# Kernel tuning notes

Measured on AMD Instinct MI355X. Metric: run time of the kernel, lower is better.

Reference implementation:

```python
import jax, jax.numpy as jnp
import numpy as np

HID = 256   # hidden_dim
P = 16      # pool_size
EPS = 1e-5


def _ln(x, g, b):
    m = x.mean(-1, keepdims=True)
    v = x.var(-1, keepdims=True)
    return (x - m) * jax.lax.rsqrt(v + EPS) * g + b


def setup_inputs() -> dict:
    key = jax.random.key(0)
    ks = jax.random.split(key, 12)
    B, Cf, H, W = 8, 512, 64, 64
    Cg = Cf // 2
    Co = Cf // 2
    s = 0.02
    d = {}
    d['e_f'] = jax.random.normal(ks[0], (B, Cf, H, W), jnp.float32)
    d['e_g'] = jax.random.normal(ks[1], (B, Cg, H, W), jnp.float32)
    d['l_feat'] = jax.random.normal(ks[2], (B, 768, 20), jnp.float32)
    d['l_mask'] = jnp.ones((B, 20, 1), jnp.float32)
    d['ln_f_g'] = jnp.ones((Cf,), jnp.float32)
    d['ln_f_b'] = jnp.zeros((Cf,), jnp.float32)
    d['ln_g_g'] = jnp.ones((Cg,), jnp.float32)
    d['ln_g_b'] = jnp.zeros((Cg,), jnp.float32)
    d['wq'] = jax.random.normal(ks[3], (Cf, HID), jnp.float32) * s
    d['bq'] = jnp.zeros((HID,), jnp.float32)
    d['wk'] = jax.random.normal(ks[4], (Cg, HID), jnp.float32) * s
    d['bk'] = jnp.zeros((HID,), jnp.float32)
    d['wv'] = jax.random.normal(ks[5], (Cg, HID), jnp.float32) * s
    d['bv'] = jnp.zeros((HID,), jnp.float32)
    d['wo'] = jax.random.normal(ks[6], (HID, HID), jnp.float32) * s
    d['bo'] = jnp.zeros((HID,), jnp.float32)
    d['dw_k'] = jax.random.normal(ks[7], (HID, 1, 3, 3), jnp.float32) * s  # depthwise kernel (OIHW, I=1)
    d['efp_w'] = jax.random.normal(ks[8], (HID, Cf), jnp.float32) * s     # 1x1 conv v_channels->hidden
    d['efp_b'] = jnp.zeros((HID,), jnp.float32)
    d['outc_w'] = jax.random.normal(ks[9], (Co, HID), jnp.float32) * s    # 1x1 conv hidden->out
    d['outc_b'] = jnp.zeros((Co,), jnp.float32)
    d['bn_g'] = jnp.ones((Co,), jnp.float32)
    d['bn_b'] = jnp.zeros((Co,), jnp.float32)
    d['bn_m'] = jnp.zeros((Co,), jnp.float32)
    d['bn_v'] = jnp.ones((Co,), jnp.float32)
    return d


def reference(e_f, e_g, l_feat, l_mask, ln_f_g, ln_f_b, ln_g_g, ln_g_b,
              wq, bq, wk, bk, wv, bv, wo, bo, dw_k, efp_w, efp_b,
              outc_w, outc_b, bn_g, bn_b, bn_m, bn_v):
    B, Cf, H, W = e_f.shape
    # Q = w_qi(LN(e_f))                                  (B, HW, HID)
    q = _ln(e_f.transpose(0, 2, 3, 1), ln_f_g, ln_f_b).reshape(B, H * W, Cf) @ wq + bq
    # K/V projections from LN(e_g)
    g = _ln(e_g.transpose(0, 2, 3, 1), ln_g_g, ln_g_b).reshape(B, H * W, -1)
    k = (g @ wk + bk).reshape(B, H, W, HID)
    v = (g @ wv + bv).reshape(B, H, W, HID)
    # 16x16 max/avg pooling -> (B, Hp*Wp, HID)
    k = jnp.max(k.reshape(B, H // P, P, W // P, P, HID), axis=(2, 4)).reshape(B, -1, HID)
    v = jnp.mean(v.reshape(B, H // P, P, W // P, P, HID), axis=(2, 4)).reshape(B, -1, HID)
    # pooled attention
    attn = jax.nn.softmax(jnp.einsum('bqd,bkd->bqk', q, k) * (HID ** -0.5), axis=-1)
    a_i = jnp.einsum('bqk,bkd->bqd', attn, v)  # (B, HW, HID)
    # depthwise 3x3 conv on Q (NCHW)
    q_nchw = q.reshape(B, H, W, HID).transpose(0, 3, 1, 2)
    dw = jax.lax.conv_general_dilated(q_nchw, dw_k, (1, 1), [(1, 1), (1, 1)],
                                      feature_group_count=HID)
    combined = dw + a_i.reshape(B, H, W, HID).transpose(0, 3, 1, 2)
    comb = combined.transpose(0, 2, 3, 1).reshape(B, H * W, HID) @ wo + bo
    comb = comb.reshape(B, H, W, HID).transpose(0, 3, 1, 2)
    # 1x1 proj of e_f, elementwise gate
    efp = jnp.einsum('bchw,oc->bohw', e_f, efp_w) + efp_b[None, :, None, None]
    e_a = efp * comb
    # out: 1x1 conv + BN (inference) + ReLU (dropout inactive in eval)
    out = jnp.einsum('bchw,oc->bohw', e_a, outc_w) + outc_b[None, :, None, None]
    scale = (bn_g * jax.lax.rsqrt(bn_v + EPS))[None, :, None, None]
    out = (out - bn_m[None, :, None, None]) * scale + bn_b[None, :, None, None]
    return jax.nn.relu(out)
```

## Files before the change

### kernel.cpp

```cpp
#include <hip/hip_runtime.h>
#include <math.h>

#define EPS 1e-5f

typedef __attribute__((ext_vector_type(8))) short bf16x8;
typedef __attribute__((ext_vector_type(4))) float f32x4;

__device__ __forceinline__ unsigned short f2bf(float f) {
    unsigned int u = __float_as_uint(f);
    u += 0x7fff + ((u >> 16) & 1);
    return (unsigned short)(u >> 16);
}
__device__ __forceinline__ float bf2f(unsigned short h) {
    return __uint_as_float(((unsigned int)h) << 16);
}
__device__ __forceinline__ float lof(unsigned int u) {
    return __uint_as_float(u << 16);
}
__device__ __forceinline__ float hif(unsigned int u) {
    return __uint_as_float(u & 0xffff0000u);
}
__device__ __forceinline__ void async16(void* lds, const void* g) {
    __builtin_amdgcn_global_load_lds(
        (const __attribute__((address_space(1))) unsigned int*)g,
        (__attribute__((address_space(3))) unsigned int*)lds, 16, 0, 0);
}

__global__ __launch_bounds__(256) void prep_all(
    const float* __restrict__ lnfg, const float* __restrict__ lnfb,
    const float* __restrict__ wq, const float* __restrict__ bq,
    const float* __restrict__ efpw, const float* __restrict__ efpb,
    const float* __restrict__ lngg, const float* __restrict__ lngb,
    const float* __restrict__ wk, const float* __restrict__ bk,
    const float* __restrict__ wv, const float* __restrict__ bv,
    const float* __restrict__ wo, const float* __restrict__ outcw,
    const float* __restrict__ outcb, const float* __restrict__ bng,
    const float* __restrict__ bnb, const float* __restrict__ bnm,
    const float* __restrict__ bnv, const float* __restrict__ dwk,
    unsigned short* __restrict__ Wb1t, unsigned short* __restrict__ Wb2t,
    unsigned short* __restrict__ Wot, unsigned short* __restrict__ Woc,
    float* __restrict__ dwt,
    float* __restrict__ cs1, float* __restrict__ cst1,
    float* __restrict__ cs2, float* __restrict__ cst2,
    float* __restrict__ scv, float* __restrict__ shv)
{
    int idx = blockIdx.x * 256 + threadIdx.x;
    if (idx < 262144) {
        int n = idx >> 9, k = idx & 511;
        float v = (n < 256) ? lnfg[k] * wq[k * 256 + n]
                            : efpw[(size_t)(n - 256) * 512 + k];
        Wb1t[idx] = f2bf(v);
    } else if (idx < 327680) {
        int j = idx - 262144; int n = j >> 8, k = j & 255;
        Wb2t[j] = f2bf(lngg[k] * wk[k * 256 + n]);
    } else if (idx < 393216) {
        int j = idx - 327680; int n = j >> 8, k = j & 255;
        Wot[j] = f2bf(wo[k * 256 + n]);
    } else if (idx < 458752) {
        int j = idx - 393216;
        Woc[j] = f2bf(outcw[j]);
    } else if (idx < 461056) {
        int j = idx - 458752; int tap = j >> 8, ch = j & 255;
        dwt[j] = dwk[ch * 9 + tap];
    } else if (idx < 462336) {
        int j = idx - 461056;
        if (j < 256) {
            int n = j; float cs = 0.f, ct = 0.f;
            for (int k = 0; k < 512; k++) {
                float w = wq[k * 256 + n];
                cs += lnfg[k] * w; ct += lnfb[k] * w;
            }
            cs1[n] = cs; cst1[n] = ct + bq[n];
        } else if (j < 512) {
            cs1[j] = 0.f; cst1[j] = efpb[j - 256];
        } else if (j < 768) {
            int n = j - 512; float cs = 0.f, ct = 0.f;
            for (int k = 0; k < 256; k++) {
                float w = wk[k * 256 + n];
                cs += lngg[k] * w; ct += lngb[k] * w;
            }
            cs2[n] = cs; cst2[n] = ct + bk[n];
        } else if (j < 1024) {
            int n = j - 768; float cs = 0.f, ct = 0.f;
            for (int k = 0; k < 256; k++) {
                float w = wv[k * 256 + n];
                cs += lngg[k] * w; ct += lngb[k] * w;
            }
            cs2[256 + n] = cs; cst2[256 + n] = ct + bv[n];
        } else {
            int n = j - 1024;
            float s = bng[n] * rsqrtf(bnv[n] + EPS);
            scv[n] = s;
            shv[n] = (outcb[n] - bnm[n]) * s + bnb[n];
        }
    }
}

__global__ __launch_bounds__(256) void transpose_fg(
    const float* __restrict__ ef, const float* __restrict__ eg,
    unsigned short* __restrict__ ef_bf, unsigned short* __restrict__ eg_bf,
    float* __restrict__ pf, float* __restrict__ pfq,
    float* __restrict__ pg, float* __restrict__ pgq)
{
    __shared__ float tile[64][65];
    __shared__ float psum[4][64], pss[4][64];
    int id = blockIdx.x;
    const float* src; unsigned short* dst; float* ps; float* pq;
    int C, cblk, b, p0;
    if (id < 2048) {
        src = ef; dst = ef_bf; ps = pf; pq = pfq; C = 512;
        b = id >> 8; cblk = (id >> 5) & 7; p0 = (id & 31) * 128;
    } else {
        id -= 2048;
        src = eg; dst = eg_bf; ps = pg; pq = pgq; C = 256;
        b = id >> 7; cblk = (id >> 5) & 3; p0 = (id & 31) * 128;
    }
    int c0 = cblk * 64;
    const float* s = src + ((size_t)b * C + c0) * 4096 + p0;
    int t = threadIdx.x;
    int cr = t >> 4, p4 = (t & 15) * 4;
    int lane = t & 63, grp = t >> 6;
    int pr = t >> 3, c8 = (t & 7) * 8;

    float4 r1[4], r2[4];
#pragma unroll
    for (int i = 0; i < 4; i++)
        r1[i] = *(const float4*)(s + (size_t)(i * 16 + cr) * 4096 + p4);
#pragma unroll
    for (int i = 0; i < 4; i++)
        r2[i] = *(const float4*)(s + (size_t)(i * 16 + cr) * 4096 + 64 + p4);

#pragma unroll
    for (int half = 0; half < 2; half++) {
#pragma unroll
        for (int i = 0; i < 4; i++) {
            float4 v = half ? r2[i] : r1[i];
            int c = i * 16 + cr;
            tile[c][p4 + 0] = v.x; tile[c][p4 + 1] = v.y;
            tile[c][p4 + 2] = v.z; tile[c][p4 + 3] = v.w;
        }
        __syncthreads();

        int pbase = p0 + half * 64;
        unsigned short* d = dst + ((size_t)(b * 4096 + pbase)) * C + c0;
#pragma unroll
        for (int i = 0; i < 2; i++) {
            int p = i * 32 + pr;
            uint4 pk;
            pk.x = (unsigned)f2bf(tile[c8 + 0][p]) | ((unsigned)f2bf(tile[c8 + 1][p]) << 16);
            pk.y = (unsigned)f2bf(tile[c8 + 2][p]) | ((unsigned)f2bf(tile[c8 + 3][p]) << 16);
            pk.z = (unsigned)f2bf(tile[c8 + 4][p]) | ((unsigned)f2bf(tile[c8 + 5][p]) << 16);
            pk.w = (unsigned)f2bf(tile[c8 + 6][p]) | ((unsigned)f2bf(tile[c8 + 7][p]) << 16);
            *(uint4*)(d + (size_t)p * C + c8) = pk;
        }

        float sm = 0.f, sq = 0.f;
#pragma unroll
        for (int j = 0; j < 16; j++) {
            float v = tile[grp * 16 + j][lane];
            sm += v; sq += v * v;
        }
        psum[grp][lane] = sm; pss[grp][lane] = sq;
        __syncthreads();
        if (t < 64) {
            float fs = psum[0][t] + psum[1][t] + psum[2][t] + psum[3][t];
            float fq = pss[0][t] + pss[1][t] + pss[2][t] + pss[3][t];
            ps[cblk * 32768 + b * 4096 + pbase + t] = fs;
            pq[cblk * 32768 + b * 4096 + pbase + t] = fq;
        }
        if (half == 0) __syncthreads();
    }
}

__global__ __launch_bounds__(256) void ln_finalize(
    const float* __restrict__ pf, const float* __restrict__ pfq,
    const float* __restrict__ pg, const float* __restrict__ pgq,
    float* __restrict__ mf, float* __restrict__ rf,
    float* __restrict__ mg, float* __restrict__ rg)
{
    int gp = blockIdx.x * 256 + threadIdx.x;
    float s = 0.f, q = 0.f;
#pragma unroll
    for (int i = 0; i < 8; i++) { s += pf[i * 32768 + gp]; q += pfq[i * 32768 + gp]; }
    float m = s * (1.f / 512.f);
    float v = q * (1.f / 512.f) - m * m;
    mf[gp] = m; rf[gp] = rsqrtf(v + EPS);
    s = 0.f; q = 0.f;
#pragma unroll
    for (int i = 0; i < 4; i++) { s += pg[i * 32768 + gp]; q += pgq[i * 32768 + gp]; }
    m = s * (1.f / 256.f);
    v = q * (1.f / 256.f) - m * m;
    mg[gp] = m; rg[gp] = rsqrtf(v + EPS);
}

template<int K>
__device__ __forceinline__ void mfma_core(
    const unsigned short* __restrict__ A, const unsigned short* __restrict__ Bt,
    int m0, int n0, unsigned short* As, unsigned short* Bs, f32x4 acc[4][4])
{
    const int tid = threadIdx.x;
    const int wave = tid >> 6, lane = tid & 63;
    const int wm = (wave & 1) * 64, wn = (wave >> 1) * 64;
#pragma unroll
    for (int i = 0; i < 4; i++)
#pragma unroll
        for (int j = 0; j < 4; j++) acc[i][j] = (f32x4){0.f, 0.f, 0.f, 0.f};

    const int srow = wave * 32 + (lane >> 3);
    const int sg = (lane & 7) ^ ((lane >> 3) & 7);
    const unsigned short* ga = A + (size_t)(m0 + srow) * K + sg * 8;
    const unsigned short* gb = Bt + (size_t)(n0 + srow) * K + sg * 8;

    for (int k0 = 0; k0 < K; k0 += 64) {
#pragma unroll
        for (int t = 0; t < 4; t++) {
            async16(As + (wave * 32 + t * 8) * 64, ga + (size_t)t * 8 * K + k0);
            async16(Bs + (wave * 32 + t * 8) * 64, gb + (size_t)t * 8 * K + k0);
        }
        __syncthreads();
#pragma unroll
        for (int ks = 0; ks < 2; ks++) {
            bf16x8 af[4], bfr[4];
            int kb = ks * 4 + (lane >> 4);
            int slot = (kb ^ (lane & 7)) * 8;
#pragma unroll
            for (int i = 0; i < 4; i++) {
                int m = wm + i * 16 + (lane & 15);
                af[i] = *(const bf16x8*)&As[m * 64 + slot];
                int n = wn + i * 16 + (lane & 15);
                bfr[i] = *(const bf16x8*)&Bs[n * 64 + slot];
            }
#pragma unroll
            for (int i = 0; i < 4; i++)
#pragma unroll
                for (int j = 0; j < 4; j++)
                    acc[i][j] = __builtin_amdgcn_mfma_f32_16x16x32_bf16(
                        af[i], bfr[j], acc[i][j], 0, 0, 0);
        }
        __syncthreads();
    }
}

__global__ __launch_bounds__(256, 2) void gemm1_mfma(
    const unsigned short* __restrict__ ef_bf, const unsigned short* __restrict__ Wb1t,
    const float* __restrict__ cs1, const float* __restrict__ cst1,
    const float* __restrict__ mf, const float* __restrict__ rf,
    unsigned short* __restrict__ qbuf, unsigned short* __restrict__ efpbuf)
{
    __shared__ unsigned short As[128 * 64];
    __shared__ unsigned short Bs[256 * 64];
    f32x4 acc[4][8];
    const int tid = threadIdx.x;
    const int wave = tid >> 6, lane = tid & 63;
    const int wm = (wave & 1) * 64, wn = (wave >> 1) * 128;
    const int m0 = blockIdx.x * 128, n0 = blockIdx.y * 256;
#pragma unroll
    for (int i = 0; i < 4; i++)
#pragma unroll
        for (int j = 0; j < 8; j++) acc[i][j] = (f32x4){0.f, 0.f, 0.f, 0.f};

    const int srow = lane >> 3;
    const int sg = (lane & 7) ^ (srow & 7);
    const unsigned short* ga = ef_bf + (size_t)(m0 + wave * 32 + srow) * 512 + sg * 8;
    const unsigned short* gb = Wb1t + (size_t)(n0 + wave * 64 + srow) * 512 + sg * 8;

    for (int k0 = 0; k0 < 512; k0 += 64) {
#pragma unroll
        for (int t = 0; t < 4; t++)
            async16(As + (wave * 32 + t * 8) * 64, ga + (size_t)t * 8 * 512 + k0);
#pragma unroll
        for (int t = 0; t < 8; t++)
            async16(Bs + (wave * 64 + t * 8) * 64, gb + (size_t)t * 8 * 512 + k0);
        __syncthreads();
#pragma unroll
        for (int ks = 0; ks < 2; ks++) {
            bf16x8 af[4], bfr[8];
            int kb = ks * 4 + (lane >> 4);
            int slot = (kb ^ (lane & 7)) * 8;
#pragma unroll
            for (int i = 0; i < 4; i++)
                af[i] = *(const bf16x8*)&As[(wm + i * 16 + (lane & 15)) * 64 + slot];
#pragma unroll
            for (int j = 0; j < 8; j++)
                bfr[j] = *(const bf16x8*)&Bs[(wn + j * 16 + (lane & 15)) * 64 + slot];
#pragma unroll
            for (int i = 0; i < 4; i++)
#pragma unroll
                for (int j = 0; j < 8; j++)
                    acc[i][j] = __builtin_amdgcn_mfma_f32_16x16x32_bf16(
                        af[i], bfr[j], acc[i][j], 0, 0, 0);
        }
        __syncthreads();
    }

    bool isq = (n0 == 0);
#pragma unroll
    for (int i = 0; i < 4; i++) {
#pragma unroll
        for (int r = 0; r < 4; r++) {
            int gm = m0 + wm + i * 16 + ((lane >> 4) * 4) + r;
            float mean = mf[gm], rs = rf[gm];
#pragma unroll
            for (int j = 0; j < 8; j++) {
                int nn = wn + j * 16 + (lane & 15);
                float v = acc[i][j][r];
                if (isq) {
                    int n = nn;
                    float o = rs * (v - mean * cs1[n]) + cst1[n];
                    qbuf[(size_t)gm * 256 + nn] = f2bf(o);
                } else {
                    int n = nn + 256;
                    efpbuf[(size_t)gm * 256 + nn] = f2bf(v + cst1[n]);
                }
            }
        }
    }
}

__global__ __launch_bounds__(256) void gemm2k_mfma(
    const unsigned short* __restrict__ eg_bf, const unsigned short* __restrict__ Wb2t,
    const float* __restrict__ cs2, const float* __restrict__ cst2,
    const float* __restrict__ mg, const float* __restrict__ rg,
    unsigned short* __restrict__ kfull)
{
    __shared__ unsigned short As[8192], Bs[8192];
    f32x4 acc[4][4];
    int m0 = blockIdx.x * 128, n0 = blockIdx.y * 128;
    mfma_core<256>(eg_bf, Wb2t, m0, n0, As, Bs, acc);
    int lane = threadIdx.x & 63, wave = threadIdx.x >> 6;
    int wm = (wave & 1) * 64, wn = (wave >> 1) * 64;
#pragma unroll
    for (int i = 0; i < 4; i++) {
#pragma unroll
        for (int r = 0; r < 4; r++) {
            int gm = m0 + wm + i * 16 + ((lane >> 4) * 4) + r;
            float mean = mg[gm], rs = rg[gm];
#pragma unroll
            for (int j = 0; j < 4; j++) {
                int n = n0 + wn + j * 16 + (lane & 15);
                float o = rs * (acc[i][j][r] - mean * cs2[n]) + cst2[n];
                kfull[(size_t)gm * 256 + n] = f2bf(o);
            }
        }
    }
}

__global__ __launch_bounds__(256) void gemm34_mfma(
    const unsigned short* __restrict__ comb, const unsigned short* __restrict__ Wot,
    const float* __restrict__ bo, const unsigned short* __restrict__ efp,
    const unsigned short* __restrict__ Woc,
    const float* __restrict__ scv, const float* __restrict__ shv,
    float* __restrict__ outp)
{
    __shared__ unsigned short As[64 * 64];
    __shared__ unsigned short Bs[256 * 64];
    __shared__ unsigned short eat[64 * 256];
    const int tid = threadIdx.x;
    const int wave = tid >> 6, lane = tid & 63;
    const int m0 = blockIdx.x * 64;

    const int srow = lane >> 3;
    const int sg = (lane & 7) ^ (srow & 7);

    f32x4 acc[4][4];
#pragma unroll
    for (int i = 0; i < 4; i++)
#pragma unroll
        for (int j = 0; j < 4; j++) acc[i][j] = (f32x4){0.f, 0.f, 0.f, 0.f};

    const unsigned short* ga = comb + (size_t)(m0 + wave * 16 + srow) * 256 + sg * 8;
    const unsigned short* gb = Wot + (size_t)(wave * 64 + srow) * 256 + sg * 8;

    for (int k0 = 0; k0 < 256; k0 += 64) {
#pragma unroll
        for (int t = 0; t < 2; t++)
            async16(As + (wave * 16 + t * 8) * 64, ga + (size_t)t * 8 * 256 + k0);
#pragma unroll
        for (int t = 0; t < 8; t++)
            async16(Bs + (wave * 64 + t * 8) * 64, gb + (size_t)t * 8 * 256 + k0);
        __syncthreads();
#pragma unroll
        for (int ks = 0; ks < 2; ks++) {
            bf16x8 af[4], bfr[4];
            int kb = ks * 4 + (lane >> 4);
            int slot = (kb ^ (lane & 7)) * 8;
#pragma unroll
            for (int i = 0; i < 4; i++) {
                af[i]  = *(const bf16x8*)&As[(i * 16 + (lane & 15)) * 64 + slot];
                bfr[i] = *(const bf16x8*)&Bs[(wave * 64 + i * 16 + (lane & 15)) * 64 + slot];
            }
#pragma unroll
            for (int i = 0; i < 4; i++)
#pragma unroll
                for (int j = 0; j < 4; j++)
                    acc[i][j] = __builtin_amdgcn_mfma_f32_16x16x32_bf16(
                        af[i], bfr[j], acc[i][j], 0, 0, 0);
        }
        __syncthreads();
    }

    float bo4[4];
#pragma unroll
    for (int j = 0; j < 4; j++) bo4[j] = bo[wave * 64 + j * 16 + (lane & 15)];
#pragma unroll
    for (int i = 0; i < 4; i++) {
#pragma unroll
        for (int r = 0; r < 4; r++) {
            int pos = i * 16 + ((lane >> 4) * 4) + r;
#pragma unroll
            for (int j = 0; j < 4; j++) {
                int n = wave * 64 + j * 16 + (lane & 15);
                float o = (acc[i][j][r] + bo4[j])
                          * bf2f(efp[(size_t)(m0 + pos) * 256 + n]);
                int o8 = j * 2 + ((lane >> 3) & 1);
                int slot = o8 ^ (pos & 7);
                eat[pos * 256 + wave * 64 + slot * 8 + (lane & 7)] = f2bf(o);
            }
        }
    }

    f32x4 acc2[4][4];
#pragma unroll
    for (int i = 0; i < 4; i++)
#pragma unroll
        for (int j = 0; j < 4; j++) acc2[i][j] = (f32x4){0.f, 0.f, 0.f, 0.f};

    const unsigned short* gw = Woc + (size_t)(wave * 64 + srow) * 256 + sg * 8;
    for (int k0 = 0; k0 < 256; k0 += 64) {
#pragma unroll
        for (int t = 0; t < 8; t++)
            async16(Bs + (wave * 64 + t * 8) * 64, gw + (size_t)t * 8 * 256 + k0);
        __syncthreads();
        int kc = k0 >> 6;
#pragma unroll
        for (int ks = 0; ks < 2; ks++) {
            bf16x8 af2[4], bf2_[4];
            int kb = ks * 4 + (lane >> 4);
            int slot = (kb ^ (lane & 7)) * 8;
#pragma unroll
            for (int i = 0; i < 4; i++) {
                af2[i]  = *(const bf16x8*)&Bs[(wave * 64 + i * 16 + (lane & 15)) * 64 + slot];
                bf2_[i] = *(const bf16x8*)&eat[(i * 16 + (lane & 15)) * 256 + kc * 64 + slot];
            }
#pragma unroll
            for (int i = 0; i < 4; i++)
#pragma unroll
                for (int j = 0; j < 4; j++)
                    acc2[i][j] = __builtin_amdgcn_mfma_f32_16x16x32_bf16(
                        af2[i], bf2_[j], acc2[i][j], 0, 0, 0);
        }
        __syncthreads();
    }

#pragma unroll
    for (int i = 0; i < 4; i++) {
#pragma unroll
        for (int r = 0; r < 4; r++) {
            int co = wave * 64 + i * 16 + ((lane >> 4) * 4) + r;
            float s = scv[co], hh = shv[co];
#pragma unroll
            for (int j = 0; j < 4; j++) {
                int p = m0 + j * 16 + (lane & 15);
                float o = fmaxf(fmaf(acc2[i][j][r], s, hh), 0.f);
                outp[((size_t)(p >> 12)) * 1048576 + (size_t)co * 4096 + (p & 4095)] = o;
            }
        }
    }
}

__global__ __launch_bounds__(256) void pool_phase(
    const unsigned short* __restrict__ kfull, const float* __restrict__ eg,
    const float* __restrict__ rg, const float* __restrict__ mg,
    unsigned short* __restrict__ kpb, float* __restrict__ s1,
    float* __restrict__ s0)
{
    __shared__ float smem[4352];
    int id = blockIdx.x;
    int t = threadIdx.x;
    if (id < 128) {
        int b = id >> 4, cell = id & 15;
        int hp = cell >> 2, wp = cell & 3;
        int g8 = t & 31, rr = t >> 5;
        float kmx[8];
#pragma unroll
        for (int j = 0; j < 8; j++) kmx[j] = -3.402823466e38f;
#pragma unroll
        for (int rsub = 0; rsub < 2; rsub++) {
            int r = rr * 2 + rsub;
            int prow = (hp * 16 + r) * 64 + wp * 16;
            for (int cl = 0; cl < 16; cl++) {
                size_t basei = ((size_t)(b * 4096 + prow + cl)) * 256 + g8 * 8;
                uint4 kv = *(const uint4*)(kfull + basei);
                kmx[0] = fmaxf(kmx[0], lof(kv.x)); kmx[1] = fmaxf(kmx[1], hif(kv.x));
                kmx[2] = fmaxf(kmx[2], lof(kv.y)); kmx[3] = fmaxf(kmx[3], hif(kv.y));
                kmx[4] = fmaxf(kmx[4], lof(kv.z)); kmx[5] = fmaxf(kmx[5], hif(kv.z));
                kmx[6] = fmaxf(kmx[6], lof(kv.w)); kmx[7] = fmaxf(kmx[7], hif(kv.w));
            }
        }
#pragma unroll
        for (int j = 0; j < 8; j++) smem[rr * 256 + g8 * 8 + j] = kmx[j];
        __syncthreads();
        float m = smem[t];
#pragma unroll
        for (int r2 = 1; r2 < 8; r2++) m = fmaxf(m, smem[r2 * 256 + t]);
        kpb[(size_t)(b * 16 + cell) * 256 + t] = f2bf(m);
    } else {
        int id2 = id - 128;
        int b = id2 >> 6, hp = (id2 >> 4) & 3, cgrp = id2 & 15;
        int rr = t >> 4, cq = t & 15, cx = cq >> 2;
        int p = (hp * 16 + rr) * 64 + cq * 4;
        float4 w4 = *(const float4*)&rg[b * 4096 + p];
        float part[16];
        const float* egb = eg + ((size_t)b * 256 + cgrp * 16) * 4096 + p;
#pragma unroll
        for (int cc = 0; cc < 16; cc++) {
            float4 v4 = *(const float4*)(egb + (size_t)cc * 4096);
            part[cc] = w4.x * v4.x + w4.y * v4.y + w4.z * v4.z + w4.w * v4.w;
        }
#pragma unroll
        for (int cc = 0; cc < 16; cc++) smem[t * 16 + cc] = part[cc];
        if (cgrp == 0) {
            float4 m4 = *(const float4*)&mg[b * 4096 + p];
            smem[4096 + t] = w4.x * m4.x + w4.y * m4.y + w4.z * m4.z + w4.w * m4.w;
        }
        __syncthreads();
        if (t < 64) {
            int cx2 = t >> 4, cc = t & 15;
            float sacc = 0.f;
#pragma unroll
            for (int rr2 = 0; rr2 < 16; rr2++)
#pragma unroll
                for (int dq = 0; dq < 4; dq++)
                    sacc += smem[(rr2 * 16 + cx2 * 4 + dq) * 16 + cc];
            s1[((size_t)(b * 16 + hp * 4 + cx2)) * 256 + cgrp * 16 + cc] = sacc;
        }
        if (cgrp == 0 && t < 4) {
            float sacc = 0.f;
#pragma unroll
            for (int rr2 = 0; rr2 < 16; rr2++)
#pragma unroll
                for (int dq = 0; dq < 4; dq++)
                    sacc += smem[4096 + rr2 * 16 + t * 4 + dq];
            s0[b * 16 + hp * 4 + t] = sacc;
        }
    }
}

__global__ __launch_bounds__(256) void vpool_gemm(
    const float* __restrict__ s1, const float* __restrict__ s0,
    const float* __restrict__ lngg, const float* __restrict__ wv,
    const float* __restrict__ cs2, const float* __restrict__ cst2,
    float* __restrict__ vp)
{
    int cell = blockIdx.x;
    int n = threadIdx.x;
    const float* s1r = s1 + (size_t)cell * 256;
    float acc = 0.f;
    for (int c = 0; c < 256; c++)
        acc = fmaf(lngg[c] * s1r[c], wv[c * 256 + n], acc);
    vp[(size_t)cell * 256 + n] = acc * (1.f / 256.f)
        - (s0[cell] * (1.f / 256.f)) * cs2[256 + n] + cst2[256 + n];
}

__global__ __launch_bounds__(256) void combined_dw(
    const unsigned short* __restrict__ qbuf, const unsigned short* __restrict__ kpb,
    const float* __restrict__ vp, const float* __restrict__ dwt,
    unsigned short* __restrict__ combined)
{
    __shared__ float attns[256];
    int wave = threadIdx.x >> 6, lane = threadIdx.x & 63;
    int id = blockIdx.x;
    int b = id & 7, seg = id >> 3;
    int pidx0 = seg * 16;

    if (wave == 0) {
        int fr = lane & 15, quad = lane >> 4;
        const unsigned short* qrow = qbuf + (size_t)(b * 4096 + pidx0 + fr) * 256 + quad * 8;
        const unsigned short* krow = kpb + (size_t)(b * 16 + fr) * 256 + quad * 8;
        f32x4 sacc = {0.f, 0.f, 0.f, 0.f};
#pragma unroll
        for (int ks = 0; ks < 8; ks++) {
            bf16x8 af = *(const bf16x8*)(qrow + ks * 32);
            bf16x8 bf_ = *(const bf16x8*)(krow + ks * 32);
            sacc = __builtin_amdgcn_mfma_f32_16x16x32_bf16(af, bf_, sacc, 0, 0, 0);
        }
#pragma unroll
        for (int r = 0; r < 4; r++) {
            float s = sacc[r] * 0.0625f;
            float mx = s;
#pragma unroll
            for (int off = 8; off >= 1; off >>= 1) mx = fmaxf(mx, __shfl_xor(mx, off));
            float e = __expf(s - mx);
            float sum = e;
#pragma unroll
            for (int off = 8; off >= 1; off >>= 1) sum += __shfl_xor(sum, off);
            attns[(quad * 4 + r) * 16 + fr] = e / sum;
        }
    }
    __syncthreads();

    int pidx = pidx0 + wave * 4;
    int h = pidx >> 6, w0 = pidx & 63;
    int o4 = lane * 4;

    float4 kreg[9];
#pragma unroll
    for (int tap = 0; tap < 9; tap++)
        kreg[tap] = *(const float4*)&dwt[tap * 256 + o4];

    float4 acc[4];
#pragma unroll
    for (int i = 0; i < 4; i++) acc[i] = (float4){0.f, 0.f, 0.f, 0.f};

    const float* arow = attns + (wave * 4) * 16;
#pragma unroll
    for (int c = 0; c < 16; c++) {
        float4 v = *(const float4*)&vp[(size_t)(b * 16 + c) * 256 + o4];
#pragma unroll
        for (int i = 0; i < 4; i++) {
            float a = arow[i * 16 + c];
            acc[i].x = fmaf(a, v.x, acc[i].x); acc[i].y = fmaf(a, v.y, acc[i].y);
            acc[i].z = fmaf(a, v.z, acc[i].z); acc[i].w = fmaf(a, v.w, acc[i].w);
        }
    }
#pragma unroll
    for (int dy = 0; dy < 3; dy++) {
        int hh = h + dy - 1;
        if (hh < 0 || hh > 63) continue;
        const unsigned short* qr = qbuf + ((size_t)(b * 4096 + hh * 64)) * 256;
        float4 ft[6];
#pragma unroll
        for (int c = 0; c < 6; c++) {
            int xx = w0 - 1 + c;
            if (xx < 0 || xx > 63) {
                ft[c] = (float4){0.f, 0.f, 0.f, 0.f};
            } else {
                uint2 qa = *(const uint2*)(qr + (size_t)xx * 256 + o4);
                ft[c] = (float4){lof(qa.x), hif(qa.x), lof(qa.y), hif(qa.y)};
            }
        }
#pragma unroll
        for (int dx = 0; dx < 3; dx++) {
            float4 kk = kreg[dy * 3 + dx];
#pragma unroll
            for (int i = 0; i < 4; i++) {
                float4 qv = ft[i + dx];
                acc[i].x = fmaf(qv.x, kk.x, acc[i].x);
                acc[i].y = fmaf(qv.y, kk.y, acc[i].y);
                acc[i].z = fmaf(qv.z, kk.z, acc[i].z);
                acc[i].w = fmaf(qv.w, kk.w, acc[i].w);
            }
        }
    }
#pragma unroll
    for (int i = 0; i < 4; i++) {
        uint2 pk;
        pk.x = (unsigned)f2bf(acc[i].x) | ((unsigned)f2bf(acc[i].y) << 16);
        pk.y = (unsigned)f2bf(acc[i].z) | ((unsigned)f2bf(acc[i].w) << 16);
        *(uint2*)(combined + ((size_t)(b * 4096 + pidx + i)) * 256 + o4) = pk;
    }
}

extern "C" void kernel_launch(void* const* d_in, const int* in_sizes, int n_in,
                              void* d_out, int out_size, void* d_ws, size_t ws_size,
                              hipStream_t stream)
{
    const float* e_f   = (const float*)d_in[0];
    const float* e_g   = (const float*)d_in[1];
    const float* lnfg  = (const float*)d_in[4];
    const float* lnfb  = (const float*)d_in[5];
    const float* lngg  = (const float*)d_in[6];
    const float* lngb  = (const float*)d_in[7];
    const float* wq    = (const float*)d_in[8];
    const float* bq    = (const float*)d_in[9];
    const float* wk    = (const float*)d_in[10];
    const float* bk    = (const float*)d_in[11];
    const float* wv    = (const float*)d_in[12];
    const float* bv    = (const float*)d_in[13];
    const float* wo    = (const float*)d_in[14];
    const float* bo    = (const float*)d_in[15];
    const float* dwk   = (const float*)d_in[16];
    const float* efpw  = (const float*)d_in[17];
    const float* efpb  = (const float*)d_in[18];
    const float* outcw = (const float*)d_in[19];
    const float* outcb = (const float*)d_in[20];
    const float* bng   = (const float*)d_in[21];
    const float* bnb   = (const float*)d_in[22];
    const float* bnm   = (const float*)d_in[23];
    const float* bnv   = (const float*)d_in[24];
    float* outp = (float*)d_out;

    char* base = (char*)d_ws;
    auto alloc = [&](size_t bytes) -> char* {
        char* r = base; base += (bytes + 255) & ~(size_t)255; return r;
    };
    float* pf    = (float*)alloc(8 * 32768 * 4);
    float* pfq   = (float*)alloc(8 * 32768 * 4);
    float* pg    = (float*)alloc(4 * 32768 * 4);
    float* pgq   = (float*)alloc(4 * 32768 * 4);
    float* mf    = (float*)alloc(32768 * 4);
    float* rf    = (float*)alloc(32768 * 4);
    float* mg    = (float*)alloc(32768 * 4);
    float* rg    = (float*)alloc(32768 * 4);
    float* cs1   = (float*)alloc(512 * 4);
    float* cst1  = (float*)alloc(512 * 4);
    float* cs2   = (float*)alloc(512 * 4);
    float* cst2  = (float*)alloc(512 * 4);
    float* scv   = (float*)alloc(256 * 4);
    float* shv   = (float*)alloc(256 * 4);
    float* dwt   = (float*)alloc(9 * 256 * 4);
    unsigned short* Wb1t = (unsigned short*)alloc(262144 * 2);
    unsigned short* Wb2t = (unsigned short*)alloc(65536 * 2);
    unsigned short* Wot  = (unsigned short*)alloc(65536 * 2);
    unsigned short* Woc  = (unsigned short*)alloc(65536 * 2);
    unsigned short* ef_bf = (unsigned short*)alloc((size_t)32768 * 512 * 2);
    unsigned short* eg_bf = (unsigned short*)alloc((size_t)32768 * 256 * 2);
    unsigned short* qbuf  = (unsigned short*)alloc((size_t)32768 * 256 * 2);
    unsigned short* efpbuf = (unsigned short*)alloc((size_t)32768 * 256 * 2);
    unsigned short* kfull = (unsigned short*)alloc((size_t)32768 * 256 * 2);
    unsigned short* kpb  = (unsigned short*)alloc(128 * 256 * 2);
    float* vp    = (float*)alloc(128 * 256 * 4);
    float* s1    = (float*)alloc(128 * 256 * 4);
    float* s0    = (float*)alloc(128 * 4);

    prep_all<<<1806, 256, 0, stream>>>(
        lnfg, lnfb, wq, bq, efpw, efpb, lngg, lngb, wk, bk, wv, bv, wo,
        outcw, outcb, bng, bnb, bnm, bnv, dwk,
        Wb1t, Wb2t, Wot, Woc, dwt, cs1, cst1, cs2, cst2, scv, shv);
    transpose_fg<<<3072, 256, 0, stream>>>(e_f, e_g, ef_bf, eg_bf,
                                           pf, pfq, pg, pgq);
    ln_finalize<<<128, 256, 0, stream>>>(pf, pfq, pg, pgq, mf, rf, mg, rg);
    gemm1_mfma<<<dim3(256, 2), 256, 0, stream>>>(ef_bf, Wb1t, cs1, cst1, mf, rf,
                                                 qbuf, efpbuf);
    gemm2k_mfma<<<dim3(256, 2), 256, 0, stream>>>(eg_bf, Wb2t, cs2, cst2, mg, rg,
                                                  kfull);
    pool_phase<<<640, 256, 0, stream>>>(kfull, e_g, rg, mg, kpb, s1, s0);
    vpool_gemm<<<128, 256, 0, stream>>>(s1, s0, lngg, wv, cs2, cst2, vp);
    combined_dw<<<2048, 256, 0, stream>>>(qbuf, kpb, vp, dwt, kfull);
    gemm34_mfma<<<512, 256, 0, stream>>>(kfull, Wot, bo, efpbuf,
                                         Woc, scv, shv, outp);
}
```

Baseline: 316.7 us.

## Enlarge transpose tiles and fold LN finalize into GEMM prologues

The transpose/stats kernel now handles 64 channels by 256 pixels per block in a single 64KB rotated-swizzle LDS tile. This halves the block count and lets each thread produce a complete per-pixel partial sum without the cross-wave reduction. The separate ln_finalize launch is removed; gemm1 and gemm2k each reduce the channel-block partials for their 128 rows into shared memory at kernel start. gemm2k also writes mg/rg for the later pool phase. Risks are lower occupancy from the large LDS tile and redundant finalize work across the two N-blocks of each GEMM.

```diff
diff --git a/kernel.cpp b/kernel.cpp
--- a/kernel.cpp
+++ b/kernel.cpp
@@ -102,95 +102,70 @@
     float* __restrict__ pf, float* __restrict__ pfq,
     float* __restrict__ pg, float* __restrict__ pgq)
 {
-    __shared__ float tile[64][65];
-    __shared__ float psum[4][64], pss[4][64];
+    __shared__ float tile[16384];
     int id = blockIdx.x;
     const float* src; unsigned short* dst; float* ps; float* pq;
     int C, cblk, b, p0;
-    if (id < 2048) {
+    if (id < 1024) {
         src = ef; dst = ef_bf; ps = pf; pq = pfq; C = 512;
-        b = id >> 8; cblk = (id >> 5) & 7; p0 = (id & 31) * 128;
+        b = id >> 7; cblk = (id >> 4) & 7; p0 = (id & 15) * 256;
     } else {
-        id -= 2048;
+        id -= 1024;
         src = eg; dst = eg_bf; ps = pg; pq = pgq; C = 256;
-        b = id >> 7; cblk = (id >> 5) & 3; p0 = (id & 31) * 128;
+        b = id >> 6; cblk = (id >> 4) & 3; p0 = (id & 15) * 256;
     }
     int c0 = cblk * 64;
     const float* s = src + ((size_t)b * C + c0) * 4096 + p0;
     int t = threadIdx.x;
-    int cr = t >> 4, p4 = (t & 15) * 4;
-    int lane = t & 63, grp = t >> 6;
+    int wave = t >> 6, lane = t & 63;
+
+    float4 rr[16];
+#pragma unroll
+    for (int i = 0; i < 16; i++) {
+        int c = wave * 16 + i;
+        rr[i] = *(const float4*)(s + (size_t)c * 4096 + lane * 4);
+    }
+#pragma unroll
+    for (int i = 0; i < 16; i++) {
+        int c = wave * 16 + i;
+        int rq = (c + (c >> 3)) & 63;
+        *(float4*)&tile[c * 256 + (((lane + rq) & 63) << 2)] = rr[i];
+    }
+    __syncthreads();
+
+    {
+        int pq4 = t >> 2, pr4 = t & 3;
+        float sm = 0.f, sq = 0.f;
+#pragma unroll
+        for (int c = 0; c < 64; c++) {
+            int rq = (c + (c >> 3)) & 63;
+            float v = tile[c * 256 + (((pq4 + rq) & 63) << 2) + pr4];
+            sm += v; sq += v * v;
+        }
+        ps[cblk * 32768 + b * 4096 + p0 + t] = sm;
+        pq[cblk * 32768 + b * 4096 + p0 + t] = sq;
+    }
+
+    unsigned short* d = dst + ((size_t)(b * 4096 + p0)) * C + c0;
     int pr = t >> 3, c8 = (t & 7) * 8;
-
-    float4 r1[4], r2[4];
-#pragma unroll
-    for (int i = 0; i < 4; i++)
-        r1[i] = *(const float4*)(s + (size_t)(i * 16 + cr) * 4096 + p4);
-#pragma unroll
-    for (int i = 0; i < 4; i++)
-        r2[i] = *(const float4*)(s + (size_t)(i * 16 + cr) * 4096 + 64 + p4);
-
-#pragma unroll
-    for (int half = 0; half < 2; half++) {
-#pragma unroll
-        for (int i = 0; i < 4; i++) {
-            float4 v = half ? r2[i] : r1[i];
-            int c = i * 16 + cr;
-            tile[c][p4 + 0] = v.x; tile[c][p4 + 1] = v.y;
-            tile[c][p4 + 2] = v.z; tile[c][p4 + 3] = v.w;
-        }
-        __syncthreads();
-
-        int pbase = p0 + half * 64;
-        unsigned short* d = dst + ((size_t)(b * 4096 + pbase)) * C + c0;
-#pragma unroll
-        for (int i = 0; i < 2; i++) {
-            int p = i * 32 + pr;
-            uint4 pk;
-            pk.x = (unsigned)f2bf(tile[c8 + 0][p]) | ((unsigned)f2bf(tile[c8 + 1][p]) << 16);
-            pk.y = (unsigned)f2bf(tile[c8 + 2][p]) | ((unsigned)f2bf(tile[c8 + 3][p]) << 16);
-            pk.z = (unsigned)f2bf(tile[c8 + 4][p]) | ((unsigned)f2bf(tile[c8 + 5][p]) << 16);
-            pk.w = (unsigned)f2bf(tile[c8 + 6][p]) | ((unsigned)f2bf(tile[c8 + 7][p]) << 16);
-            *(uint4*)(d + (size_t)p * C + c8) = pk;
-        }
-
-        float sm = 0.f, sq = 0.f;
-#pragma unroll
-        for (int j = 0; j < 16; j++) {
-            float v = tile[grp * 16 + j][lane];
-            sm += v; sq += v * v;
-        }
-        psum[grp][lane] = sm; pss[grp][lane] = sq;
-        __syncthreads();
-        if (t < 64) {
-            float fs = psum[0][t] + psum[1][t] + psum[2][t] + psum[3][t];
-            float fq = pss[0][t] + pss[1][t] + pss[2][t] + pss[3][t];
-            ps[cblk * 32768 + b * 4096 + pbase + t] = fs;
-            pq[cblk * 32768 + b * 4096 + pbase + t] = fq;
-        }
-        if (half == 0) __syncthreads();
-    }
-}
-
-__global__ __launch_bounds__(256) void ln_finalize(
-    const float* __restrict__ pf, const float* __restrict__ pfq,
-    const float* __restrict__ pg, const float* __restrict__ pgq,
-    float* __restrict__ mf, float* __restrict__ rf,
-    float* __restrict__ mg, float* __restrict__ rg)
-{
-    int gp = blockIdx.x * 256 + threadIdx.x;
-    float s = 0.f, q = 0.f;
-#pragma unroll
-    for (int i = 0; i < 8; i++) { s += pf[i * 32768 + gp]; q += pfq[i * 32768 + gp]; }
-    float m = s * (1.f / 512.f);
-    float v = q * (1.f / 512.f) - m * m;
-    mf[gp] = m; rf[gp] = rsqrtf(v + EPS);
-    s = 0.f; q = 0.f;
-#pragma unroll
-    for (int i = 0; i < 4; i++) { s += pg[i * 32768 + gp]; q += pgq[i * 32768 + gp]; }
-    m = s * (1.f / 256.f);
-    v = q * (1.f / 256.f) - m * m;
-    mg[gp] = m; rg[gp] = rsqrtf(v + EPS);
+#pragma unroll
+    for (int i = 0; i < 8; i++) {
+        int p = i * 32 + pr;
+        int pq4 = p >> 2, pr4 = p & 3;
+        float v[8];
+#pragma unroll
+        for (int j = 0; j < 8; j++) {
+            int c = c8 + j;
+            int rq = (c + (c >> 3)) & 63;
+            v[j] = tile[c * 256 + (((pq4 + rq) & 63) << 2) + pr4];
+        }
+        uint4 pk;
+        pk.x = (unsigned)f2bf(v[0]) | ((unsigned)f2bf(v[1]) << 16);
+        pk.y = (unsigned)f2bf(v[2]) | ((unsigned)f2bf(v[3]) << 16);
+        pk.z = (unsigned)f2bf(v[4]) | ((unsigned)f2bf(v[5]) << 16);
+        pk.w = (unsigned)f2bf(v[6]) | ((unsigned)f2bf(v[7]) << 16);
+        *(uint4*)(d + (size_t)p * C + c8) = pk;
+    }
 }
 
 template<int K>
@@ -244,16 +219,28 @@
 __global__ __launch_bounds__(256, 2) void gemm1_mfma(
     const unsigned short* __restrict__ ef_bf, const unsigned short* __restrict__ Wb1t,
     const float* __restrict__ cs1, const float* __restrict__ cst1,
-    const float* __restrict__ mf, const float* __restrict__ rf,
+    const float* __restrict__ pf, const float* __restrict__ pfq,
     unsigned short* __restrict__ qbuf, unsigned short* __restrict__ efpbuf)
 {
     __shared__ unsigned short As[128 * 64];
     __shared__ unsigned short Bs[256 * 64];
+    __shared__ float smf[128], srf[128];
     f32x4 acc[4][8];
     const int tid = threadIdx.x;
     const int wave = tid >> 6, lane = tid & 63;
     const int wm = (wave & 1) * 64, wn = (wave >> 1) * 128;
     const int m0 = blockIdx.x * 128, n0 = blockIdx.y * 256;
+
+    if (tid < 128) {
+        int gm = m0 + tid;
+        float s = 0.f, q = 0.f;
+#pragma unroll
+        for (int i = 0; i < 8; i++) { s += pf[i * 32768 + gm]; q += pfq[i * 32768 + gm]; }
+        float m = s * (1.f / 512.f);
+        smf[tid] = m;
+        srf[tid] = rsqrtf(q * (1.f / 512.f) - m * m + EPS);
+    }
+
 #pragma unroll
     for (int i = 0; i < 4; i++)
 #pragma unroll
@@ -298,8 +285,9 @@
     for (int i = 0; i < 4; i++) {
 #pragma unroll
         for (int r = 0; r < 4; r++) {
-            int gm = m0 + wm + i * 16 + ((lane >> 4) * 4) + r;
-            float mean = mf[gm], rs = rf[gm];
+            int lm = wm + i * 16 + ((lane >> 4) * 4) + r;
+            int gm = m0 + lm;
+            float mean = smf[lm], rs = srf[lm];
 #pragma unroll
             for (int j = 0; j < 8; j++) {
                 int nn = wn + j * 16 + (lane & 15);
@@ -320,21 +308,37 @@
 __global__ __launch_bounds__(256) void gemm2k_mfma(
     const unsigned short* __restrict__ eg_bf, const unsigned short* __restrict__ Wb2t,
     const float* __restrict__ cs2, const float* __restrict__ cst2,
-    const float* __restrict__ mg, const float* __restrict__ rg,
+    const float* __restrict__ pg, const float* __restrict__ pgq,
+    float* __restrict__ mg, float* __restrict__ rg,
     unsigned short* __restrict__ kfull)
 {
     __shared__ unsigned short As[8192], Bs[8192];
+    __shared__ float smg[128], srg[128];
     f32x4 acc[4][4];
     int m0 = blockIdx.x * 128, n0 = blockIdx.y * 128;
+    int tid = threadIdx.x;
+
+    if (tid < 128) {
+        int gm = m0 + tid;
+        float s = 0.f, q = 0.f;
+#pragma unroll
+        for (int i = 0; i < 4; i++) { s += pg[i * 32768 + gm]; q += pgq[i * 32768 + gm]; }
+        float m = s * (1.f / 256.f);
+        float r = rsqrtf(q * (1.f / 256.f) - m * m + EPS);
+        smg[tid] = m; srg[tid] = r;
+        if (n0 == 0) { mg[gm] = m; rg[gm] = r; }
+    }
+
     mfma_core<256>(eg_bf, Wb2t, m0, n0, As, Bs, acc);
-    int lane = threadIdx.x & 63, wave = threadIdx.x >> 6;
+    int lane = tid & 63, wave = tid >> 6;
     int wm = (wave & 1) * 64, wn = (wave >> 1) * 64;
 #pragma unroll
     for (int i = 0; i < 4; i++) {
 #pragma unroll
         for (int r = 0; r < 4; r++) {
-            int gm = m0 + wm + i * 16 + ((lane >> 4) * 4) + r;
-            float mean = mg[gm], rs = rg[gm];
+            int lm = wm + i * 16 + ((lane >> 4) * 4) + r;
+            int gm = m0 + lm;
+            float mean = smg[lm], rs = srg[lm];
 #pragma unroll
             for (int j = 0; j < 4; j++) {
                 int n = n0 + wn + j * 16 + (lane & 15);
@@ -698,8 +702,6 @@
     float* pfq   = (float*)alloc(8 * 32768 * 4);
     float* pg    = (float*)alloc(4 * 32768 * 4);
     float* pgq   = (float*)alloc(4 * 32768 * 4);
-    float* mf    = (float*)alloc(32768 * 4);
-    float* rf    = (float*)alloc(32768 * 4);
     float* mg    = (float*)alloc(32768 * 4);
     float* rg    = (float*)alloc(32768 * 4);
     float* cs1   = (float*)alloc(512 * 4);
@@ -727,13 +729,12 @@
         lnfg, lnfb, wq, bq, efpw, efpb, lngg, lngb, wk, bk, wv, bv, wo,
         outcw, outcb, bng, bnb, bnm, bnv, dwk,
         Wb1t, Wb2t, Wot, Woc, dwt, cs1, cst1, cs2, cst2, scv, shv);
-    transpose_fg<<<3072, 256, 0, stream>>>(e_f, e_g, ef_bf, eg_bf,
+    transpose_fg<<<1536, 256, 0, stream>>>(e_f, e_g, ef_bf, eg_bf,
                                            pf, pfq, pg, pgq);
-    ln_finalize<<<128, 256, 0, stream>>>(pf, pfq, pg, pgq, mf, rf, mg, rg);
-    gemm1_mfma<<<dim3(256, 2), 256, 0, stream>>>(ef_bf, Wb1t, cs1, cst1, mf, rf,
+    gemm1_mfma<<<dim3(256, 2), 256, 0, stream>>>(ef_bf, Wb1t, cs1, cst1, pf, pfq,
                                                  qbuf, efpbuf);
-    gemm2k_mfma<<<dim3(256, 2), 256, 0, stream>>>(eg_bf, Wb2t, cs2, cst2, mg, rg,
-                                                  kfull);
+    gemm2k_mfma<<<dim3(256, 2), 256, 0, stream>>>(eg_bf, Wb2t, cs2, cst2, pg, pgq,
+                                                  mg, rg, kfull);
     pool_phase<<<640, 256, 0, stream>>>(kfull, e_g, rg, mg, kpb, s1, s0);
     vpool_gemm<<<128, 256, 0, stream>>>(s1, s0, lngg, wv, cs2, cst2, vp);
     combined_dw<<<2048, 256, 0, stream>>>(qbuf, kpb, vp, dwt, kfull);
```

Measured after the change: 320.5 us. About the same (+1.2%).
